# Kernel tuning notes

Measured on AMD Instinct MI355X. Metric: run time of the kernel, lower is better.

## Reference

```python
import jax, jax.numpy as jnp
import numpy as np

D_MODEL = 512
N_HEADS = 8
HEAD_DIM = D_MODEL // N_HEADS
MAX_LEN = 250  # relative table has 2*MAX_LEN-1 = 499 rows
B, L = 2, 2048


def setup_inputs() -> dict:
    rng = jax.random.key(0)
    ks = jax.random.split(rng, 10)
    w = 1.0 / np.sqrt(D_MODEL)
    return {
        "query": jax.random.normal(ks[0], (B, L, D_MODEL), jnp.float32),
        "key": jax.random.normal(ks[1], (B, L, D_MODEL), jnp.float32),
        "value": jax.random.normal(ks[2], (B, L, D_MODEL), jnp.float32),
        "mask": jax.random.randint(ks[3], (B, L), 0, 2, jnp.int32),
        # weights stored as [in, out]; apply as x @ W + b (equivalent to torch Linear)
        "Wq": jax.random.normal(ks[4], (D_MODEL, D_MODEL), jnp.float32) * w,
        "bq": jnp.zeros((D_MODEL,), jnp.float32),
        "Wk": jax.random.normal(ks[5], (D_MODEL, D_MODEL), jnp.float32) * w,
        "bk": jnp.zeros((D_MODEL,), jnp.float32),
        "Wv": jax.random.normal(ks[6], (D_MODEL, D_MODEL), jnp.float32) * w,
        "bv": jnp.zeros((D_MODEL,), jnp.float32),
        "Wo": jax.random.normal(ks[7], (D_MODEL, D_MODEL), jnp.float32) * w,
        "bo": jnp.zeros((D_MODEL,), jnp.float32),
        "rel_table": jax.random.normal(ks[8], (2 * MAX_LEN - 1, HEAD_DIM), jnp.float32),
    }


def reference(query, key, value, mask, Wq, bq, Wk, bk, Wv, bv, Wo, bo, rel_table):
    b, l, d = query.shape
    hd = d // N_HEADS

    def split_heads(x):  # [b,l,d] -> [b,h,l,hd]
        return x.reshape(b, l, N_HEADS, hd).transpose(0, 2, 1, 3)

    Q = split_heads(query @ Wq + bq)
    K = split_heads(key @ Wk + bk)
    V = split_heads(value @ Wv + bv)

    scores = jnp.einsum('bhid,bhjd->bhij', Q, K) / jnp.sqrt(jnp.float32(hd))

    # relative position indices: idx[i,j] = clamp(j - i + MAX_LEN-1, 0, 2*MAX_LEN-2)
    pos = jnp.arange(l)
    idx = jnp.clip(pos[None, :] - pos[:, None] + MAX_LEN - 1, 0, 2 * MAX_LEN - 2)
    rel = rel_table[idx]  # [l, l, hd] gather
    # Shaw-style additive relative-position bias (per-pair scalar from Q . rel)
    scores = scores + jnp.einsum('bhid,ijd->bhij', Q, rel)

    # key-padding mask: [b,l] -> [b,1,1,l]
    scores = jnp.where(mask[:, None, None, :] == 0, jnp.float32(-1e10), scores)

    weights = jax.nn.softmax(scores, axis=-1)  # [b,h,l,l]
    out = jnp.einsum('bhij,bhjd->bhid', weights, V)
    out = out.transpose(0, 2, 1, 3).reshape(b, l, d)
    return out @ Wo + bo
```

## Files before the change

kernel.cpp:

```cpp
#include <hip/hip_runtime.h>
#include <math.h>

#define NREL 499
#define NREL_PAD 504
#define LDB 72
#define LDT 72
#define KVSZ (64 * LDB)

typedef __attribute__((ext_vector_type(8))) short bf16x8;
typedef __attribute__((ext_vector_type(4))) float f32x4;

__device__ __forceinline__ float bf2f(ushort x) {
  union { unsigned u; float f; } v; v.u = ((unsigned)x) << 16; return v.f;
}
__device__ __forceinline__ ushort f2bf(float x) {
  union { float f; unsigned u; } v; v.f = x;
  return (ushort)((v.u + 0x8000u) >> 16);
}
__device__ __forceinline__ ushort f2h(float x) {
  union { _Float16 h; ushort u; } v; v.h = (_Float16)x; return v.u;
}
__device__ __forceinline__ float h2f(ushort u) {
  union { _Float16 h; ushort u; } v; v.u = u; return (float)v.h;
}
__device__ __forceinline__ bf16x8 pack8(float4 a, float4 b) {
  bf16x8 r;
  r[0] = (short)f2bf(a.x); r[1] = (short)f2bf(a.y);
  r[2] = (short)f2bf(a.z); r[3] = (short)f2bf(a.w);
  r[4] = (short)f2bf(b.x); r[5] = (short)f2bf(b.y);
  r[6] = (short)f2bf(b.z); r[7] = (short)f2bf(b.w);
  return r;
}

__global__ __launch_bounds__(256) void prep_wt(const float* __restrict__ W0,
                                               const float* __restrict__ W1,
                                               const float* __restrict__ W2,
                                               const float* __restrict__ W3,
                                               const int* __restrict__ mask,
                                               const float* __restrict__ rel,
                                               ushort* __restrict__ Wt,
                                               ushort* __restrict__ maskbf,
                                               ushort* __restrict__ rel8) {
  __shared__ float T[64][68];
  const int t = threadIdx.x;
  const int k0 = blockIdx.x * 64, n0 = blockIdx.y * 64, z = blockIdx.z;
  const float* W = (z == 0) ? W0 : (z == 1) ? W1 : (z == 2) ? W2 : W3;
#pragma unroll
  for (int s = 0; s < 4; ++s) {
    int idx = t + s * 256;
    int r = idx >> 4, c4 = (idx & 15) << 2;
    *(float4*)&T[r][c4] = *(const float4*)(W + (size_t)(k0 + r) * 512 + n0 + c4);
  }
  if (blockIdx.x == 0 && blockIdx.y == 0) {
    int base = z * 1024 + t * 4;
    int4 mv = *(const int4*)(mask + base);
    ushort4 mo;
    mo.x = mv.x ? 0x3F80 : 0; mo.y = mv.y ? 0x3F80 : 0;
    mo.z = mv.z ? 0x3F80 : 0; mo.w = mv.w ? 0x3F80 : 0;
    *(ushort4*)(maskbf + base) = mo;
  } else if (blockIdx.x == 1 && blockIdx.y == 0) {
    int base = z * 8192 + t * 32;
#pragma unroll
    for (int c = 0; c < 4; ++c) {
      int e0 = base + c * 8;
      ushort tmp[8];
#pragma unroll
      for (int k = 0; k < 8; ++k) {
        int e = e0 + k;
        float v = (e < NREL * 64) ? rel[e] * 8.f : 0.f;
        tmp[k] = f2bf(v);
      }
      *(ushort4*)(rel8 + e0) = make_ushort4(tmp[0], tmp[1], tmp[2], tmp[3]);
      *(ushort4*)(rel8 + e0 + 4) = make_ushort4(tmp[4], tmp[5], tmp[6], tmp[7]);
    }
  }
  __syncthreads();
#pragma unroll
  for (int s = 0; s < 4; ++s) {
    int idx = t + s * 256;
    int row = idx >> 4, c4 = (idx & 15) << 2;
    ushort4 u = make_ushort4(f2bf(T[c4 + 0][row]), f2bf(T[c4 + 1][row]),
                             f2bf(T[c4 + 2][row]), f2bf(T[c4 + 3][row]));
    *(ushort4*)(Wt + (size_t)z * 262144 + (size_t)(n0 + row) * 512 + k0 + c4) = u;
  }
}

template <int MODE, int AFP32>
__device__ __forceinline__ void gemm_tile_body(const void* __restrict__ Av,
                                               const ushort* __restrict__ Wt,
                                               const float* __restrict__ bias,
                                               const int* __restrict__ mvec,
                                               void* __restrict__ outv,
                                               int bx, int by, float oscale) {
  __shared__ ushort As[64 * LDT];
  __shared__ ushort Bs[64 * LDT];
  const int t = threadIdx.x;
  const int lane = t & 63, wave = t >> 6;
  const int m16 = lane & 15, quad = lane >> 4;
  const int koff = quad << 3;
  const int i0 = by * 64, n0 = bx * 64;
  const int row0 = t >> 3, off0 = (t & 7) << 3;
  const int row1 = (t + 256) >> 3, off1 = ((t + 256) & 7) << 3;
  const ushort* Ab16 = (const ushort*)Av + (size_t)i0 * 512;
  const float*  Ab32 = (const float*)Av + (size_t)i0 * 512;
  const ushort* Bb = Wt + (size_t)n0 * 512;

  uint4 ar0, ar1;
  float4 af00, af01, af10, af11;
  if (AFP32) {
    af00 = *(const float4*)(Ab32 + (size_t)row0 * 512 + off0);
    af01 = *(const float4*)(Ab32 + (size_t)row0 * 512 + off0 + 4);
    af10 = *(const float4*)(Ab32 + (size_t)row1 * 512 + off1);
    af11 = *(const float4*)(Ab32 + (size_t)row1 * 512 + off1 + 4);
  } else {
    ar0 = *(const uint4*)(Ab16 + (size_t)row0 * 512 + off0);
    ar1 = *(const uint4*)(Ab16 + (size_t)row1 * 512 + off1);
  }
  uint4 br0 = *(const uint4*)(Bb + (size_t)row0 * 512 + off0);
  uint4 br1 = *(const uint4*)(Bb + (size_t)row1 * 512 + off1);

  f32x4 acc[4] = {{0.f, 0.f, 0.f, 0.f}, {0.f, 0.f, 0.f, 0.f},
                  {0.f, 0.f, 0.f, 0.f}, {0.f, 0.f, 0.f, 0.f}};

  for (int ks = 0; ks < 8; ++ks) {
    __syncthreads();
    if (AFP32) {
      *(bf16x8*)&As[row0 * LDT + off0] = pack8(af00, af01);
      *(bf16x8*)&As[row1 * LDT + off1] = pack8(af10, af11);
    } else {
      *(uint4*)&As[row0 * LDT + off0] = ar0;
      *(uint4*)&As[row1 * LDT + off1] = ar1;
    }
    *(uint4*)&Bs[row0 * LDT + off0] = br0;
    *(uint4*)&Bs[row1 * LDT + off1] = br1;
    __syncthreads();

    const int kn = ((ks + 1) & 7) << 6;
    if (AFP32) {
      af00 = *(const float4*)(Ab32 + (size_t)row0 * 512 + kn + off0);
      af01 = *(const float4*)(Ab32 + (size_t)row0 * 512 + kn + off0 + 4);
      af10 = *(const float4*)(Ab32 + (size_t)row1 * 512 + kn + off1);
      af11 = *(const float4*)(Ab32 + (size_t)row1 * 512 + kn + off1 + 4);
    } else {
      ar0 = *(const uint4*)(Ab16 + (size_t)row0 * 512 + kn + off0);
      ar1 = *(const uint4*)(Ab16 + (size_t)row1 * 512 + kn + off1);
    }
    br0 = *(const uint4*)(Bb + (size_t)row0 * 512 + kn + off0);
    br1 = *(const uint4*)(Bb + (size_t)row1 * 512 + kn + off1);

    __builtin_amdgcn_s_setprio(1);
    if (MODE != 1) {
#pragma unroll
      for (int kh = 0; kh < 2; ++kh) {
        bf16x8 af = *(const bf16x8*)&As[((wave << 4) + m16) * LDT + (kh << 5) + koff];
#pragma unroll
        for (int nt = 0; nt < 4; ++nt) {
          bf16x8 wf = *(const bf16x8*)&Bs[((nt << 4) + m16) * LDT + (kh << 5) + koff];
          acc[nt] = __builtin_amdgcn_mfma_f32_16x16x32_bf16(af, wf, acc[nt], 0, 0, 0);
        }
      }
    } else {
#pragma unroll
      for (int kh = 0; kh < 2; ++kh) {
        bf16x8 wf = *(const bf16x8*)&Bs[((wave << 4) + m16) * LDT + (kh << 5) + koff];
#pragma unroll
        for (int it = 0; it < 4; ++it) {
          bf16x8 af = *(const bf16x8*)&As[((it << 4) + m16) * LDT + (kh << 5) + koff];
          acc[it] = __builtin_amdgcn_mfma_f32_16x16x32_bf16(wf, af, acc[it], 0, 0, 0);
        }
      }
    }
    __builtin_amdgcn_s_setprio(0);
  }

  if (MODE == 0) {
    float* out = (float*)outv;
#pragma unroll
    for (int nt = 0; nt < 4; ++nt) {
      float bn = bias[n0 + (nt << 4) + m16];
#pragma unroll
      for (int r = 0; r < 4; ++r) {
        int i = i0 + (wave << 4) + (quad << 2) + r;
        out[(size_t)i * 512 + n0 + (nt << 4) + m16] = acc[nt][r] + bn;
      }
    }
  } else {
    ushort* out = (ushort*)outv;
    const int b = i0 >> 11, l0 = i0 & 2047, h = n0 >> 6;
    float4 b4 = *(const float4*)(bias + n0 + (wave << 4) + (quad << 2));
    float bb[4] = {b4.x, b4.y, b4.z, b4.w};
    float mkf[4];
#pragma unroll
    for (int it = 0; it < 4; ++it)
      mkf[it] = (mvec[b * 2048 + l0 + (it << 4) + m16] != 0) ? 1.f : 0.f;
#pragma unroll
    for (int r = 0; r < 4; ++r) {
      int d = (wave << 4) + (quad << 2) + r;
#pragma unroll
      for (int it = 0; it < 4; ++it) {
        out[((size_t)(b * 8 + h) * 64 + d) * 2048 + l0 + (it << 4) + m16] =
            f2bf((acc[it][r] + bb[r]) * mkf[it]);
      }
    }
  }
}

template <int MODE, int AFP32>
__global__ __launch_bounds__(256) void gemm_tile(const void* __restrict__ A,
                                                 const ushort* __restrict__ Wt,
                                                 const float* __restrict__ bias,
                                                 void* __restrict__ outv) {
  gemm_tile_body<MODE, AFP32>(A, Wt, bias, nullptr, outv, blockIdx.x,
                              blockIdx.y, 1.f);
}

template <int QREL>
__device__ __forceinline__ void gemm_qk128(const float* __restrict__ A,
                                           const ushort* __restrict__ Wt,
                                           const float* __restrict__ bias,
                                           ushort* __restrict__ out,
                                           const ushort* __restrict__ rel8,
                                           ushort* __restrict__ qrelh,
                                           int bx, int by, float oscale) {
  __shared__ ushort As[128 * LDT];
  __shared__ ushort Bs[64 * LDT];
  const int t = threadIdx.x;
  const int lane = t & 63, wave = t >> 6;
  const int m16 = lane & 15, quad = lane >> 4;
  const int koff = quad << 3;
  const int i0 = by * 128, n0 = bx * 64;
  const float* Ab = A + (size_t)i0 * 512;
  const ushort* Bb = Wt + (size_t)n0 * 512;

  int arow[4], acol[4];
#pragma unroll
  for (int s = 0; s < 4; ++s) {
    int idx = t + s * 256;
    arow[s] = idx >> 3;
    acol[s] = (idx & 7) << 3;
  }
  const int brow0 = t >> 3, bcol0 = (t & 7) << 3;
  const int brow1 = (t + 256) >> 3, bcol1 = ((t + 256) & 7) << 3;

  float4 afA[4], afB[4];
  uint4 br0, br1;
#pragma unroll
  for (int s = 0; s < 4; ++s) {
    afA[s] = *(const float4*)(Ab + (size_t)arow[s] * 512 + acol[s]);
    afB[s] = *(const float4*)(Ab + (size_t)arow[s] * 512 + acol[s] + 4);
  }
  br0 = *(const uint4*)(Bb + (size_t)brow0 * 512 + bcol0);
  br1 = *(const uint4*)(Bb + (size_t)brow1 * 512 + bcol1);

  f32x4 acc[2][4];
#pragma unroll
  for (int mi = 0; mi < 2; ++mi)
#pragma unroll
    for (int nt = 0; nt < 4; ++nt) acc[mi][nt] = (f32x4){0.f, 0.f, 0.f, 0.f};

  for (int ks = 0; ks < 8; ++ks) {
    __syncthreads();
#pragma unroll
    for (int s = 0; s < 4; ++s)
      *(bf16x8*)&As[arow[s] * LDT + acol[s]] = pack8(afA[s], afB[s]);
    *(uint4*)&Bs[brow0 * LDT + bcol0] = br0;
    *(uint4*)&Bs[brow1 * LDT + bcol1] = br1;
    __syncthreads();

    const int kn = ((ks + 1) & 7) << 6;
#pragma unroll
    for (int s = 0; s < 4; ++s) {
      afA[s] = *(const float4*)(Ab + (size_t)arow[s] * 512 + kn + acol[s]);
      afB[s] = *(const float4*)(Ab + (size_t)arow[s] * 512 + kn + acol[s] + 4);
    }
    br0 = *(const uint4*)(Bb + (size_t)brow0 * 512 + kn + bcol0);
    br1 = *(const uint4*)(Bb + (size_t)brow1 * 512 + kn + bcol1);

    __builtin_amdgcn_s_setprio(1);
#pragma unroll
    for (int kh = 0; kh < 2; ++kh) {
      bf16x8 af0 = *(const bf16x8*)&As[((wave << 5) + m16) * LDT + (kh << 5) + koff];
      bf16x8 af1 = *(const bf16x8*)&As[((wave << 5) + 16 + m16) * LDT + (kh << 5) + koff];
#pragma unroll
      for (int nt = 0; nt < 4; ++nt) {
        bf16x8 wf = *(const bf16x8*)&Bs[((nt << 4) + m16) * LDT + (kh << 5) + koff];
        acc[0][nt] = __builtin_amdgcn_mfma_f32_16x16x32_bf16(af0, wf, acc[0][nt], 0, 0, 0);
        acc[1][nt] = __builtin_amdgcn_mfma_f32_16x16x32_bf16(af1, wf, acc[1][nt], 0, 0, 0);
      }
    }
    __builtin_amdgcn_s_setprio(0);
  }

  const int b = i0 >> 11, l0 = i0 & 2047, h = n0 >> 6;
#pragma unroll
  for (int nt = 0; nt < 4; ++nt) {
    float bn = bias[n0 + (nt << 4) + m16];
    int d = (nt << 4) + m16;
#pragma unroll
    for (int mi = 0; mi < 2; ++mi) {
#pragma unroll
      for (int r = 0; r < 4; ++r) {
        int il = (wave << 5) + (mi << 4) + (quad << 2) + r;
        ushort qb = f2bf((acc[mi][nt][r] + bn) * oscale);
        out[((size_t)(b * 8 + h) * 2048 + l0 + il) * 64 + d] = qb;
        if (QREL) As[il * LDT + d] = qb;
      }
    }
  }

  if (QREL) {
    __asm__ volatile("s_waitcnt lgkmcnt(0)" ::: "memory");
    bf16x8 afq[2][2];
#pragma unroll
    for (int g = 0; g < 2; ++g)
#pragma unroll
      for (int kh = 0; kh < 2; ++kh)
        afq[g][kh] = *(const bf16x8*)&As[((wave << 5) + (g << 4) + m16) * LDT +
                                         (kh << 5) + koff];
    const int bh = b * 8 + h;
    for (int rc = 0; rc < 32; ++rc) {
      const ushort* rp = rel8 + (size_t)((rc << 4) + m16) * 64;
      bf16x8 wf0 = *(const bf16x8*)(rp + koff);
      bf16x8 wf1 = *(const bf16x8*)(rp + 32 + koff);
      int r = (rc << 4) + m16;
#pragma unroll
      for (int g = 0; g < 2; ++g) {
        f32x4 aq = {0.f, 0.f, 0.f, 0.f};
        aq = __builtin_amdgcn_mfma_f32_16x16x32_bf16(afq[g][0], wf0, aq, 0, 0, 0);
        aq = __builtin_amdgcn_mfma_f32_16x16x32_bf16(afq[g][1], wf1, aq, 0, 0, 0);
        if (r < NREL_PAD) {
#pragma unroll
          for (int rg = 0; rg < 4; ++rg) {
            int l = l0 + (wave << 5) + (g << 4) + (quad << 2) + rg;
            qrelh[((size_t)bh * 2048 + l) * NREL_PAD + r] = f2h(aq[rg]);
          }
        }
      }
    }
  }
}

__global__ __launch_bounds__(256) void gemm_qkv(
    const float* __restrict__ q, const float* __restrict__ k,
    const float* __restrict__ v, const ushort* __restrict__ Wt,
    const float* __restrict__ bq, const float* __restrict__ bk,
    const float* __restrict__ bv, const int* __restrict__ mask,
    const ushort* __restrict__ rel8, ushort* __restrict__ Qw,
    ushort* __restrict__ Kw, ushort* __restrict__ Vtw,
    ushort* __restrict__ qrelh) {
  const int z = blockIdx.z;
  if (z == 0) {
    gemm_qk128<1>(q, Wt, bq, Qw, rel8, qrelh, blockIdx.x, blockIdx.y, 0.125f);
  } else if (z == 1) {
    gemm_qk128<0>(k, Wt + 262144, bk, Kw, nullptr, nullptr, blockIdx.x,
                  blockIdx.y, 1.f);
  } else {
#pragma unroll
    for (int s = 0; s < 2; ++s)
      gemm_tile_body<1, 1>(v, Wt + 2 * 262144, bv, mask, (void*)Vtw,
                           blockIdx.x, blockIdx.y * 2 + s, 1.f);
  }
}

__device__ __forceinline__ void gather_qv(float qv[4][4],
                                          const ushort* __restrict__ qrow,
                                          float e_lo, float e_hi,
                                          int iq, int iw0, int j0, int quad) {
  if (j0 - iw0 >= 264) {
#pragma unroll
    for (int jt = 0; jt < 4; ++jt)
#pragma unroll
      for (int r = 0; r < 4; ++r) qv[jt][r] = e_hi;
  } else if (iw0 - j0 >= 312) {
#pragma unroll
    for (int jt = 0; jt < 4; ++jt)
#pragma unroll
      for (int r = 0; r < 4; ++r) qv[jt][r] = e_lo;
  } else {
#pragma unroll
    for (int jt = 0; jt < 4; ++jt) {
#pragma unroll
      for (int r = 0; r < 4; ++r) {
        int j = j0 + (jt << 4) + (quad << 2) + r;
        int rr = min(NREL - 1, max(0, j - iq + 249));
        qv[jt][r] = h2f(qrow[rr]);
      }
    }
  }
}

__global__ __launch_bounds__(256) void flash_attn(
    const ushort* __restrict__ Qw, const ushort* __restrict__ Kw,
    const ushort* __restrict__ Vt, const ushort* __restrict__ qrelh,
    const ushort* __restrict__ maskbf, ushort* __restrict__ attnbf) {
  __shared__ ushort QPs[64 * LDB];
  __shared__ ushort Ks[2 * KVSZ];
  __shared__ ushort Vs[2 * KVSZ];
  const int t = threadIdx.x;
  const int lane = t & 63, wave = t >> 6;
  const int m16 = lane & 15, quad = lane >> 4;
  const int koff = quad << 3;
  const int bid = ((int)blockIdx.y << 5) + (int)blockIdx.x;
  const int swz = ((bid & 7) << 6) + (bid >> 3);
  const int i0 = (swz & 31) << 6;
  const int bh = swz >> 5;
  const int b = bh >> 3, h = bh & 7;
  const ushort* Qb = Qw + (size_t)bh * 2048 * 64;
  const ushort* Kb = Kw + (size_t)bh * 2048 * 64;
  const ushort* Vb = Vt + (size_t)bh * 64 * 2048;
  const ushort* mbf = maskbf + b * 2048;
  const int iw0 = i0 + (wave << 4);
  const int iq = iw0 + m16;
  const ushort* qrow = qrelh + ((size_t)bh * 2048 + iq) * NREL_PAD;
  const float e_lo = h2f(qrow[0]), e_hi = h2f(qrow[NREL - 1]);

  const int row0 = t >> 3, off0 = (t & 7) << 3;
  const int row1 = (t + 256) >> 3, off1 = ((t + 256) & 7) << 3;

  *(uint4*)&QPs[row0 * LDB + off0] =
      *(const uint4*)(Qb + (size_t)(i0 + row0) * 64 + off0);
  *(uint4*)&QPs[row1 * LDB + off1] =
      *(const uint4*)(Qb + (size_t)(i0 + row1) * 64 + off1);

  uint4 kr0 = *(const uint4*)(Kb + (size_t)row0 * 64 + off0);
  uint4 kr1 = *(const uint4*)(Kb + (size_t)row1 * 64 + off1);
  uint4 vr0 = *(const uint4*)(Vb + (size_t)row0 * 2048 + off0);
  uint4 vr1 = *(const uint4*)(Vb + (size_t)row1 * 2048 + off1);
  __syncthreads();

  bf16x8 qa0 = *(const bf16x8*)&QPs[((wave << 4) + m16) * LDB + koff];
  bf16x8 qa1 = *(const bf16x8*)&QPs[((wave << 4) + m16) * LDB + 32 + koff];

  *(uint4*)&Ks[row0 * LDB + off0] = kr0;
  *(uint4*)&Ks[row1 * LDB + off1] = kr1;
  *(uint4*)&Vs[row0 * LDB + off0] = vr0;
  *(uint4*)&Vs[row1 * LDB + off1] = vr1;
  kr0 = *(const uint4*)(Kb + (size_t)(64 + row0) * 64 + off0);
  kr1 = *(const uint4*)(Kb + (size_t)(64 + row1) * 64 + off1);
  vr0 = *(const uint4*)(Vb + (size_t)row0 * 2048 + 64 + off0);
  vr1 = *(const uint4*)(Vb + (size_t)row1 * 2048 + 64 + off1);

  bf16x8 mfA0 = *(const bf16x8*)(mbf + koff);
  bf16x8 mfA1 = *(const bf16x8*)(mbf + 32 + koff);
  float qvA[4][4];
  gather_qv(qvA, qrow, e_lo, e_hi, iq, iw0, 0, quad);
  bf16x8 mfB0, mfB1;
  float qvB[4][4];

  float m_i = -INFINITY;
  f32x4 oacc[4];
  f32x4 lacc = {0.f, 0.f, 0.f, 0.f};
#pragma unroll
  for (int dt = 0; dt < 4; ++dt) oacc[dt] = (f32x4){0.f, 0.f, 0.f, 0.f};

  __syncthreads();

#define FLASH_STEP(CUR, NXT, QV, MF0, MF1, QN, MG0, MG1, JN1, JN2)            \
  do {                                                                        \
           \
    *(uint4*)&Ks[(NXT) + row0 * LDB + off0] = kr0;                            \
    *(uint4*)&Ks[(NXT) + row1 * LDB + off1] = kr1;                            \
    *(uint4*)&Vs[(NXT) + row0 * LDB + off0] = vr0;                            \
    *(uint4*)&Vs[(NXT) + row1 * LDB + off1] = vr1;                            \
                            \
    kr0 = *(const uint4*)(Kb + (size_t)((JN2) + row0) * 64 + off0);           \
    kr1 = *(const uint4*)(Kb + (size_t)((JN2) + row1) * 64 + off1);           \
    vr0 = *(const uint4*)(Vb + (size_t)row0 * 2048 + (JN2) + off0);           \
    vr1 = *(const uint4*)(Vb + (size_t)row1 * 2048 + (JN2) + off1);           \
                                         \
    MG0 = *(const bf16x8*)(mbf + (JN1) + koff);                               \
    MG1 = *(const bf16x8*)(mbf + (JN1) + 32 + koff);                          \
    gather_qv(QN, qrow, e_lo, e_hi, iq, iw0, (JN1), quad);                    \
                                    \
    f32x4 sacc[4];                                                            \
    __builtin_amdgcn_s_setprio(1);                                            \
    _Pragma("unroll")                                                         \
    for (int jt = 0; jt < 4; ++jt) {                                          \
      bf16x8 kf0 = *(const bf16x8*)&Ks[(CUR) + ((jt << 4) + m16) * LDB + koff]; \
      bf16x8 kf1 =                                                            \
          *(const bf16x8*)&Ks[(CUR) + ((jt << 4) + m16) * LDB + 32 + koff];   \
      f32x4 z = {QV[jt][0], QV[jt][1], QV[jt][2], QV[jt][3]};                 \
      z = __builtin_amdgcn_mfma_f32_16x16x32_bf16(kf0, qa0, z, 0, 0, 0);      \
      z = __builtin_amdgcn_mfma_f32_16x16x32_bf16(kf1, qa1, z, 0, 0, 0);      \
      sacc[jt] = z;                                                           \
    }                                                                         \
    __builtin_amdgcn_s_setprio(0);                                            \
    float t0 = fmaxf(fmaxf(sacc[0][0], sacc[0][1]),                           \
                     fmaxf(sacc[0][2], sacc[0][3]));                          \
    float t1 = fmaxf(fmaxf(sacc[1][0], sacc[1][1]),                           \
                     fmaxf(sacc[1][2], sacc[1][3]));                          \
    float t2 = fmaxf(fmaxf(sacc[2][0], sacc[2][1]),                           \
                     fmaxf(sacc[2][2], sacc[2][3]));                          \
    float t3 = fmaxf(fmaxf(sacc[3][0], sacc[3][1]),                           \
                     fmaxf(sacc[3][2], sacc[3][3]));                          \
    float mx = fmaxf(fmaxf(t0, t1), fmaxf(t2, t3));                           \
    mx = fmaxf(mx, __shfl_xor(mx, 16));                                       \
    mx = fmaxf(mx, __shfl_xor(mx, 32));                                       \
    if (__any(mx > m_i + 8.f)) {                                              \
      float mnew = fmaxf(m_i, mx);                                            \
      float al = __expf(m_i - mnew);                                          \
      m_i = mnew;                                                             \
      _Pragma("unroll")                                                       \
      for (int dt = 0; dt < 4; ++dt) {                                        \
        oacc[dt][0] *= al; oacc[dt][1] *= al;                                 \
        oacc[dt][2] *= al; oacc[dt][3] *= al;                                 \
      }                                                                       \
      lacc[0] *= al; lacc[1] *= al; lacc[2] *= al; lacc[3] *= al;             \
    }                                                                         \
    const int prow = ((wave << 4) + m16) * LDB;                               \
    _Pragma("unroll")                                                         \
    for (int jt = 0; jt < 4; ++jt) {                                          \
      ushort4 pk;                                                             \
      pk.x = f2bf(__expf(sacc[jt][0] - m_i));                                 \
      pk.y = f2bf(__expf(sacc[jt][1] - m_i));                                 \
      pk.z = f2bf(__expf(sacc[jt][2] - m_i));                                 \
      pk.w = f2bf(__expf(sacc[jt][3] - m_i));                                 \
      *(ushort4*)&QPs[prow + (jt << 4) + (quad << 2)] = pk;                   \
    }                                                                         \
    __asm__ volatile("s_waitcnt lgkmcnt(0)" ::: "memory");                    \
    bf16x8 pa0 = *(const bf16x8*)&QPs[prow + koff];                           \
    bf16x8 pa1 = *(const bf16x8*)&QPs[prow + 32 + koff];                      \
    __builtin_amdgcn_s_setprio(1);                                            \
    lacc = __builtin_amdgcn_mfma_f32_16x16x32_bf16(MF0, pa0, lacc, 0, 0, 0);  \
    lacc = __builtin_amdgcn_mfma_f32_16x16x32_bf16(MF1, pa1, lacc, 0, 0, 0);  \
    _Pragma("unroll")                                                         \
    for (int dt = 0; dt < 4; ++dt) {                                          \
      bf16x8 vf0 =                                                            \
          *(const bf16x8*)&Vs[(CUR) + ((dt << 4) + m16) * LDB + koff];        \
      bf16x8 vf1 =                                                            \
          *(const bf16x8*)&Vs[(CUR) + ((dt << 4) + m16) * LDB + 32 + koff];   \
      oacc[dt] =                                                              \
          __builtin_amdgcn_mfma_f32_16x16x32_bf16(vf0, pa0, oacc[dt], 0, 0, 0); \
      oacc[dt] =                                                              \
          __builtin_amdgcn_mfma_f32_16x16x32_bf16(vf1, pa1, oacc[dt], 0, 0, 0); \
    }                                                                         \
    __builtin_amdgcn_s_setprio(0);                                            \
    __syncthreads();             \
  } while (0)

  for (int j0 = 0; j0 < 2048; j0 += 128) {
    FLASH_STEP(0, KVSZ, qvA, mfA0, mfA1, qvB, mfB0, mfB1,
               j0 + 64, (j0 + 128) & 2047);
    FLASH_STEP(KVSZ, 0, qvB, mfB0, mfB1, qvA, mfA0, mfA1,
               (j0 + 128) & 2047, (j0 + 192) & 2047);
  }
#undef FLASH_STEP

  float inv = 1.0f / lacc[0];
  ushort* dst = attnbf + (size_t)(b * 2048 + iq) * 512 + h * 64;
#pragma unroll
  for (int dt = 0; dt < 4; ++dt) {
    ushort4 st;
    st.x = f2bf(oacc[dt][0] * inv);
    st.y = f2bf(oacc[dt][1] * inv);
    st.z = f2bf(oacc[dt][2] * inv);
    st.w = f2bf(oacc[dt][3] * inv);
    *(ushort4*)(dst + (dt << 4) + (quad << 2)) = st;
  }
}

extern "C" void kernel_launch(void* const* d_in, const int* in_sizes, int n_in,
                              void* d_out, int out_size, void* d_ws,
                              size_t ws_size, hipStream_t stream) {
  const float* query = (const float*)d_in[0];
  const float* key   = (const float*)d_in[1];
  const float* value = (const float*)d_in[2];
  const int*   mask  = (const int*)d_in[3];
  const float* Wq = (const float*)d_in[4];
  const float* bq = (const float*)d_in[5];
  const float* Wk = (const float*)d_in[6];
  const float* bk = (const float*)d_in[7];
  const float* Wv = (const float*)d_in[8];
  const float* bv = (const float*)d_in[9];
  const float* Wo = (const float*)d_in[10];
  const float* bo = (const float*)d_in[11];
  const float* rel = (const float*)d_in[12];

  char* w = (char*)d_ws;
  size_t off = 0;
  ushort* Qw  = (ushort*)(w + off); off += (size_t)16 * 2048 * 64 * 2;
  ushort* Kw  = (ushort*)(w + off); off += (size_t)16 * 2048 * 64 * 2;
  ushort* Vtw = (ushort*)(w + off); off += (size_t)16 * 64 * 2048 * 2;
  ushort* Wt  = (ushort*)(w + off); off += (size_t)4 * 512 * 512 * 2;
  ushort* qrelh = (ushort*)(w + off); off += (size_t)16 * 2048 * NREL_PAD * 2;
  ushort* attnbf = (ushort*)(w + off); off += (size_t)4096 * 512 * 2;
  ushort* maskbf = (ushort*)(w + off); off += (size_t)2 * 2048 * 2;
  ushort* rel8 = (ushort*)(w + off); off += (size_t)512 * 64 * 2;
  float* out = (float*)d_out;

  dim3 bb(256);
  hipLaunchKernelGGL(prep_wt, dim3(8, 8, 4), bb, 0, stream, Wq, Wk, Wv, Wo,
                     mask, rel, Wt, maskbf, rel8);
  hipLaunchKernelGGL(gemm_qkv, dim3(8, 32, 3), bb, 0, stream, query, key, value,
                     Wt, bq, bk, bv, mask, rel8, Qw, Kw, Vtw, qrelh);
  hipLaunchKernelGGL(flash_attn, dim3(32, 16), bb, 0, stream, Qw, Kw, Vtw,
                     qrelh, maskbf, attnbf);
  hipLaunchKernelGGL((gemm_tile<0, 0>), dim3(8, 64), bb, 0, stream, attnbf,
                     Wt + 3 * 262144, bo, (void*)out);
}
```

Before: 205.6 us.

## Software-pipeline QK^T one tile ahead of softmax and PV in flash attention

Restructures the flash-attention main loop so each step computes the QK^T scores for tile t while running softmax and the PV product for tile t-1. V gets a triple-buffered LDS ring and K stays double-buffered, with a prologue that computes the first scores and an epilogue that drains the last tile. The mask fragments are now loaded just before use instead of being carried as prefetched registers. The aim is to overlap MFMA score work with the exp and softmax VALU work. The cost is more LDS and more live registers from the two score buffers, which may lower occupancy.

```diff
diff --git a/kernel.cpp b/kernel.cpp
--- a/kernel.cpp
+++ b/kernel.cpp
@@ -395,7 +395,7 @@
     const ushort* __restrict__ maskbf, ushort* __restrict__ attnbf) {
   __shared__ ushort QPs[64 * LDB];
   __shared__ ushort Ks[2 * KVSZ];
-  __shared__ ushort Vs[2 * KVSZ];
+  __shared__ ushort Vs[3 * KVSZ];
   const int t = threadIdx.x;
   const int lane = t & 63, wave = t >> 6;
   const int m16 = lane & 15, quad = lane >> 4;
@@ -416,20 +416,20 @@
 
   const int row0 = t >> 3, off0 = (t & 7) << 3;
   const int row1 = (t + 256) >> 3, off1 = ((t + 256) & 7) << 3;
+  const int prow = ((wave << 4) + m16) * LDB;
 
   *(uint4*)&QPs[row0 * LDB + off0] =
       *(const uint4*)(Qb + (size_t)(i0 + row0) * 64 + off0);
   *(uint4*)&QPs[row1 * LDB + off1] =
       *(const uint4*)(Qb + (size_t)(i0 + row1) * 64 + off1);
-
   uint4 kr0 = *(const uint4*)(Kb + (size_t)row0 * 64 + off0);
   uint4 kr1 = *(const uint4*)(Kb + (size_t)row1 * 64 + off1);
   uint4 vr0 = *(const uint4*)(Vb + (size_t)row0 * 2048 + off0);
   uint4 vr1 = *(const uint4*)(Vb + (size_t)row1 * 2048 + off1);
   __syncthreads();
 
-  bf16x8 qa0 = *(const bf16x8*)&QPs[((wave << 4) + m16) * LDB + koff];
-  bf16x8 qa1 = *(const bf16x8*)&QPs[((wave << 4) + m16) * LDB + 32 + koff];
+  bf16x8 qa0 = *(const bf16x8*)&QPs[prow + koff];
+  bf16x8 qa1 = *(const bf16x8*)&QPs[prow + 32 + koff];
 
   *(uint4*)&Ks[row0 * LDB + off0] = kr0;
   *(uint4*)&Ks[row1 * LDB + off1] = kr1;
@@ -440,59 +440,77 @@
   vr0 = *(const uint4*)(Vb + (size_t)row0 * 2048 + 64 + off0);
   vr1 = *(const uint4*)(Vb + (size_t)row1 * 2048 + 64 + off1);
 
-  bf16x8 mfA0 = *(const bf16x8*)(mbf + koff);
-  bf16x8 mfA1 = *(const bf16x8*)(mbf + 32 + koff);
-  float qvA[4][4];
+  float qvA[4][4], qvB[4][4];
   gather_qv(qvA, qrow, e_lo, e_hi, iq, iw0, 0, quad);
-  bf16x8 mfB0, mfB1;
-  float qvB[4][4];
 
   float m_i = -INFINITY;
   f32x4 oacc[4];
   f32x4 lacc = {0.f, 0.f, 0.f, 0.f};
+  f32x4 saccA[4], saccB[4];
 #pragma unroll
   for (int dt = 0; dt < 4; ++dt) oacc[dt] = (f32x4){0.f, 0.f, 0.f, 0.f};
 
   __syncthreads();
 
-#define FLASH_STEP(CUR, NXT, QV, MF0, MF1, QN, MG0, MG1, JN1, JN2)            \
+  *(uint4*)&Ks[KVSZ + row0 * LDB + off0] = kr0;
+  *(uint4*)&Ks[KVSZ + row1 * LDB + off1] = kr1;
+  *(uint4*)&Vs[KVSZ + row0 * LDB + off0] = vr0;
+  *(uint4*)&Vs[KVSZ + row1 * LDB + off1] = vr1;
+  kr0 = *(const uint4*)(Kb + (size_t)(128 + row0) * 64 + off0);
+  kr1 = *(const uint4*)(Kb + (size_t)(128 + row1) * 64 + off1);
+  vr0 = *(const uint4*)(Vb + (size_t)row0 * 2048 + 128 + off0);
+  vr1 = *(const uint4*)(Vb + (size_t)row1 * 2048 + 128 + off1);
+  __builtin_amdgcn_s_setprio(1);
+#pragma unroll
+  for (int jt = 0; jt < 4; ++jt) {
+    bf16x8 kf0 = *(const bf16x8*)&Ks[((jt << 4) + m16) * LDB + koff];
+    bf16x8 kf1 = *(const bf16x8*)&Ks[((jt << 4) + m16) * LDB + 32 + koff];
+    f32x4 z = {qvA[jt][0], qvA[jt][1], qvA[jt][2], qvA[jt][3]};
+    z = __builtin_amdgcn_mfma_f32_16x16x32_bf16(kf0, qa0, z, 0, 0, 0);
+    z = __builtin_amdgcn_mfma_f32_16x16x32_bf16(kf1, qa1, z, 0, 0, 0);
+    saccA[jt] = z;
+  }
+  __builtin_amdgcn_s_setprio(0);
+  gather_qv(qvB, qrow, e_lo, e_hi, iq, iw0, 64, quad);
+  __syncthreads();
+
+  int kC = KVSZ, kS = 0;
+  int vP = 0, vC = KVSZ, vS = 2 * KVSZ;
+
+#define FSTEP(SC, SP, QVC, QVN, JT, DONEXT)                                   \
   do {                                                                        \
-           \
-    *(uint4*)&Ks[(NXT) + row0 * LDB + off0] = kr0;                            \
-    *(uint4*)&Ks[(NXT) + row1 * LDB + off1] = kr1;                            \
-    *(uint4*)&Vs[(NXT) + row0 * LDB + off0] = vr0;                            \
-    *(uint4*)&Vs[(NXT) + row1 * LDB + off1] = vr1;                            \
-                            \
-    kr0 = *(const uint4*)(Kb + (size_t)((JN2) + row0) * 64 + off0);           \
-    kr1 = *(const uint4*)(Kb + (size_t)((JN2) + row1) * 64 + off1);           \
-    vr0 = *(const uint4*)(Vb + (size_t)row0 * 2048 + (JN2) + off0);           \
-    vr1 = *(const uint4*)(Vb + (size_t)row1 * 2048 + (JN2) + off1);           \
-                                         \
-    MG0 = *(const bf16x8*)(mbf + (JN1) + koff);                               \
-    MG1 = *(const bf16x8*)(mbf + (JN1) + 32 + koff);                          \
-    gather_qv(QN, qrow, e_lo, e_hi, iq, iw0, (JN1), quad);                    \
-                                    \
-    f32x4 sacc[4];                                                            \
+    if (DONEXT) {      \
+      *(uint4*)&Ks[kS + row0 * LDB + off0] = kr0;                             \
+      *(uint4*)&Ks[kS + row1 * LDB + off1] = kr1;                             \
+      *(uint4*)&Vs[vS + row0 * LDB + off0] = vr0;                             \
+      *(uint4*)&Vs[vS + row1 * LDB + off1] = vr1;                             \
+      const int jn2 = (((JT) + 2) << 6) & 2047;                               \
+      kr0 = *(const uint4*)(Kb + (size_t)(jn2 + row0) * 64 + off0);           \
+      kr1 = *(const uint4*)(Kb + (size_t)(jn2 + row1) * 64 + off1);           \
+      vr0 = *(const uint4*)(Vb + (size_t)row0 * 2048 + jn2 + off0);           \
+      vr1 = *(const uint4*)(Vb + (size_t)row1 * 2048 + jn2 + off1);           \
+    }                                                                         \
+                   \
     __builtin_amdgcn_s_setprio(1);                                            \
     _Pragma("unroll")                                                         \
     for (int jt = 0; jt < 4; ++jt) {                                          \
-      bf16x8 kf0 = *(const bf16x8*)&Ks[(CUR) + ((jt << 4) + m16) * LDB + koff]; \
+      bf16x8 kf0 = *(const bf16x8*)&Ks[kC + ((jt << 4) + m16) * LDB + koff];  \
       bf16x8 kf1 =                                                            \
-          *(const bf16x8*)&Ks[(CUR) + ((jt << 4) + m16) * LDB + 32 + koff];   \
-      f32x4 z = {QV[jt][0], QV[jt][1], QV[jt][2], QV[jt][3]};                 \
+          *(const bf16x8*)&Ks[kC + ((jt << 4) + m16) * LDB + 32 + koff];      \
+      f32x4 z = {QVC[jt][0], QVC[jt][1], QVC[jt][2], QVC[jt][3]};             \
       z = __builtin_amdgcn_mfma_f32_16x16x32_bf16(kf0, qa0, z, 0, 0, 0);      \
       z = __builtin_amdgcn_mfma_f32_16x16x32_bf16(kf1, qa1, z, 0, 0, 0);      \
-      sacc[jt] = z;                                                           \
+      SC[jt] = z;                                                             \
     }                                                                         \
     __builtin_amdgcn_s_setprio(0);                                            \
-    float t0 = fmaxf(fmaxf(sacc[0][0], sacc[0][1]),                           \
-                     fmaxf(sacc[0][2], sacc[0][3]));                          \
-    float t1 = fmaxf(fmaxf(sacc[1][0], sacc[1][1]),                           \
-                     fmaxf(sacc[1][2], sacc[1][3]));                          \
-    float t2 = fmaxf(fmaxf(sacc[2][0], sacc[2][1]),                           \
-                     fmaxf(sacc[2][2], sacc[2][3]));                          \
-    float t3 = fmaxf(fmaxf(sacc[3][0], sacc[3][1]),                           \
-                     fmaxf(sacc[3][2], sacc[3][3]));                          \
+    if (DONEXT)                                                               \
+      gather_qv(QVN, qrow, e_lo, e_hi, iq, iw0, (((JT) + 1) << 6) & 2047,     \
+                quad);                                                        \
+              \
+    float t0 = fmaxf(fmaxf(SP[0][0], SP[0][1]), fmaxf(SP[0][2], SP[0][3]));   \
+    float t1 = fmaxf(fmaxf(SP[1][0], SP[1][1]), fmaxf(SP[1][2], SP[1][3]));   \
+    float t2 = fmaxf(fmaxf(SP[2][0], SP[2][1]), fmaxf(SP[2][2], SP[2][3]));   \
+    float t3 = fmaxf(fmaxf(SP[3][0], SP[3][1]), fmaxf(SP[3][2], SP[3][3]));   \
     float mx = fmaxf(fmaxf(t0, t1), fmaxf(t2, t3));                           \
     mx = fmaxf(mx, __shfl_xor(mx, 16));                                       \
     mx = fmaxf(mx, __shfl_xor(mx, 32));                                       \
@@ -507,44 +525,94 @@
       }                                                                       \
       lacc[0] *= al; lacc[1] *= al; lacc[2] *= al; lacc[3] *= al;             \
     }                                                                         \
-    const int prow = ((wave << 4) + m16) * LDB;                               \
     _Pragma("unroll")                                                         \
     for (int jt = 0; jt < 4; ++jt) {                                          \
       ushort4 pk;                                                             \
-      pk.x = f2bf(__expf(sacc[jt][0] - m_i));                                 \
-      pk.y = f2bf(__expf(sacc[jt][1] - m_i));                                 \
-      pk.z = f2bf(__expf(sacc[jt][2] - m_i));                                 \
-      pk.w = f2bf(__expf(sacc[jt][3] - m_i));                                 \
+      pk.x = f2bf(__expf(SP[jt][0] - m_i));                                   \
+      pk.y = f2bf(__expf(SP[jt][1] - m_i));                                   \
+      pk.z = f2bf(__expf(SP[jt][2] - m_i));                                   \
+      pk.w = f2bf(__expf(SP[jt][3] - m_i));                                   \
       *(ushort4*)&QPs[prow + (jt << 4) + (quad << 2)] = pk;                   \
     }                                                                         \
     __asm__ volatile("s_waitcnt lgkmcnt(0)" ::: "memory");                    \
     bf16x8 pa0 = *(const bf16x8*)&QPs[prow + koff];                           \
     bf16x8 pa1 = *(const bf16x8*)&QPs[prow + 32 + koff];                      \
+    const int jp = ((JT) - 1) << 6;                                           \
+    bf16x8 mp0 = *(const bf16x8*)(mbf + jp + koff);                           \
+    bf16x8 mp1 = *(const bf16x8*)(mbf + jp + 32 + koff);                      \
     __builtin_amdgcn_s_setprio(1);                                            \
-    lacc = __builtin_amdgcn_mfma_f32_16x16x32_bf16(MF0, pa0, lacc, 0, 0, 0);  \
-    lacc = __builtin_amdgcn_mfma_f32_16x16x32_bf16(MF1, pa1, lacc, 0, 0, 0);  \
+    lacc = __builtin_amdgcn_mfma_f32_16x16x32_bf16(mp0, pa0, lacc, 0, 0, 0);  \
+    lacc = __builtin_amdgcn_mfma_f32_16x16x32_bf16(mp1, pa1, lacc, 0, 0, 0);  \
     _Pragma("unroll")                                                         \
     for (int dt = 0; dt < 4; ++dt) {                                          \
-      bf16x8 vf0 =                                                            \
-          *(const bf16x8*)&Vs[(CUR) + ((dt << 4) + m16) * LDB + koff];        \
+      bf16x8 vf0 = *(const bf16x8*)&Vs[vP + ((dt << 4) + m16) * LDB + koff];  \
       bf16x8 vf1 =                                                            \
-          *(const bf16x8*)&Vs[(CUR) + ((dt << 4) + m16) * LDB + 32 + koff];   \
+          *(const bf16x8*)&Vs[vP + ((dt << 4) + m16) * LDB + 32 + koff];      \
       oacc[dt] =                                                              \
           __builtin_amdgcn_mfma_f32_16x16x32_bf16(vf0, pa0, oacc[dt], 0, 0, 0); \
       oacc[dt] =                                                              \
           __builtin_amdgcn_mfma_f32_16x16x32_bf16(vf1, pa1, oacc[dt], 0, 0, 0); \
     }                                                                         \
     __builtin_amdgcn_s_setprio(0);                                            \
-    __syncthreads();             \
+    __syncthreads();                                                          \
+    { int tv = vP; vP = vC; vC = vS; vS = tv; }                               \
+    { int tk = kC; kC = kS; kS = tk; }                                        \
   } while (0)
 
-  for (int j0 = 0; j0 < 2048; j0 += 128) {
-    FLASH_STEP(0, KVSZ, qvA, mfA0, mfA1, qvB, mfB0, mfB1,
-               j0 + 64, (j0 + 128) & 2047);
-    FLASH_STEP(KVSZ, 0, qvB, mfB0, mfB1, qvA, mfA0, mfA1,
-               (j0 + 128) & 2047, (j0 + 192) & 2047);
-  }
-#undef FLASH_STEP
+  for (int tt = 1; tt <= 29; tt += 2) {
+    FSTEP(saccB, saccA, qvB, qvA, tt, 1);
+    FSTEP(saccA, saccB, qvA, qvB, tt + 1, 1);
+  }
+  FSTEP(saccB, saccA, qvB, qvA, 31, 0);
+
+  {
+    float t0 = fmaxf(fmaxf(saccB[0][0], saccB[0][1]),
+                     fmaxf(saccB[0][2], saccB[0][3]));
+    float t1 = fmaxf(fmaxf(saccB[1][0], saccB[1][1]),
+                     fmaxf(saccB[1][2], saccB[1][3]));
+    float t2 = fmaxf(fmaxf(saccB[2][0], saccB[2][1]),
+                     fmaxf(saccB[2][2], saccB[2][3]));
+    float t3 = fmaxf(fmaxf(saccB[3][0], saccB[3][1]),
+                     fmaxf(saccB[3][2], saccB[3][3]));
+    float mx = fmaxf(fmaxf(t0, t1), fmaxf(t2, t3));
+    mx = fmaxf(mx, __shfl_xor(mx, 16));
+    mx = fmaxf(mx, __shfl_xor(mx, 32));
+    if (__any(mx > m_i + 8.f)) {
+      float mnew = fmaxf(m_i, mx);
+      float al = __expf(m_i - mnew);
+      m_i = mnew;
+#pragma unroll
+      for (int dt = 0; dt < 4; ++dt) {
+        oacc[dt][0] *= al; oacc[dt][1] *= al;
+        oacc[dt][2] *= al; oacc[dt][3] *= al;
+      }
+      lacc[0] *= al; lacc[1] *= al; lacc[2] *= al; lacc[3] *= al;
+    }
+#pragma unroll
+    for (int jt = 0; jt < 4; ++jt) {
+      ushort4 pk;
+      pk.x = f2bf(__expf(saccB[jt][0] - m_i));
+      pk.y = f2bf(__expf(saccB[jt][1] - m_i));
+      pk.z = f2bf(__expf(saccB[jt][2] - m_i));
+      pk.w = f2bf(__expf(saccB[jt][3] - m_i));
+      *(ushort4*)&QPs[prow + (jt << 4) + (quad << 2)] = pk;
+    }
+    __asm__ volatile("s_waitcnt lgkmcnt(0)" ::: "memory");
+    bf16x8 pa0 = *(const bf16x8*)&QPs[prow + koff];
+    bf16x8 pa1 = *(const bf16x8*)&QPs[prow + 32 + koff];
+    bf16x8 mp0 = *(const bf16x8*)(mbf + 31 * 64 + koff);
+    bf16x8 mp1 = *(const bf16x8*)(mbf + 31 * 64 + 32 + koff);
+    lacc = __builtin_amdgcn_mfma_f32_16x16x32_bf16(mp0, pa0, lacc, 0, 0, 0);
+    lacc = __builtin_amdgcn_mfma_f32_16x16x32_bf16(mp1, pa1, lacc, 0, 0, 0);
+#pragma unroll
+    for (int dt = 0; dt < 4; ++dt) {
+      bf16x8 vf0 = *(const bf16x8*)&Vs[vP + ((dt << 4) + m16) * LDB + koff];
+      bf16x8 vf1 = *(const bf16x8*)&Vs[vP + ((dt << 4) + m16) * LDB + 32 + koff];
+      oacc[dt] = __builtin_amdgcn_mfma_f32_16x16x32_bf16(vf0, pa0, oacc[dt], 0, 0, 0);
+      oacc[dt] = __builtin_amdgcn_mfma_f32_16x16x32_bf16(vf1, pa1, oacc[dt], 0, 0, 0);
+    }
+  }
+#undef FSTEP
 
   float inv = 1.0f / lacc[0];
   ushort* dst = attnbf + (size_t)(b * 2048 + iq) * 512 + h * 64;
```

After: 207.7 us. About the same (+1.1%).
